# Kernel optimization log

Measured on AMD Instinct MI355X. Metric: run time of the kernel, lower is better.

## Reference

```python
import jax, jax.numpy as jnp
import numpy as np

N = 1_000_000
D = 128
S = 16384


def setup_inputs() -> dict:
    key = jax.random.key(0)
    k_x, k_idx, k_w, k_b = jax.random.split(key, 4)
    x = jax.random.normal(k_x, (N, D), dtype=jnp.float32)
    index = jnp.sort(jax.random.randint(k_idx, (N,), 0, S, dtype=jnp.int64))
    # single plain Linear layer of PyG MLP([D, D], plain_last=True)
    lim = 1.0 / np.sqrt(D)
    W = jax.random.uniform(k_w, (D, D), dtype=jnp.float32, minval=-lim, maxval=lim)
    b = jax.random.uniform(k_b, (D,), dtype=jnp.float32, minval=-lim, maxval=lim)
    return {"x": x, "W": W, "b": b, "index": index, "num_segments": S}


def reference(x, W, b, index, num_segments):
    # att = MLP(x): single plain linear layer (no activation, plain_last=True)
    att = x @ W.T + b  # [N, D]
    # segment softmax over nodes within each graph, per channel (PyG softmax)
    seg_max = jax.ops.segment_max(att, index, num_segments=num_segments)  # [S, D]
    e = jnp.exp(att - seg_max[index])  # [N, D]
    seg_sum = jax.ops.segment_sum(e, index, num_segments=num_segments)  # [S, D]
    att = e / (seg_sum[index] + 1e-16)  # [N, D]
    # attention-weighted global add pool
    return jax.ops.segment_sum(x * att, index, num_segments=num_segments)  # [S, D]
```

## Files before the change

### kernel.cpp

```cpp
#include <hip/hip_runtime.h>
#include <hip/hip_bf16.h>

#define SEGS   16384
#define DCH    128
#define CHUNK  32
#define SEGPB  4
#define FPITCH 132
#define XHBLK  520
#define LOG2E  1.4426950408889634f

using f32x4  = __attribute__((ext_vector_type(4))) float;
using bf16x8 = __attribute__((ext_vector_type(8))) short;
using u32x2  = __attribute__((ext_vector_type(2))) unsigned int;
using u32x4  = __attribute__((ext_vector_type(4))) unsigned int;

__device__ __forceinline__ float u2f(unsigned int u) { return __uint_as_float(u); }
__device__ __forceinline__ unsigned int f2u(float f) { return __float_as_uint(f); }

__global__ void setup_kernel(const float* __restrict__ W,
                             const int* __restrict__ index, int N,
                             unsigned short* __restrict__ WfH,
                             int* __restrict__ seg_start) {
  int i = blockIdx.x * blockDim.x + threadIdx.x;
  if (i < DCH * DCH) {
    int n = i >> 7, k = i & 127;
    float w = W[i] * LOG2E;
    unsigned int u = f2u(w);
    unsigned int r = (u + 0x7FFFu + ((u >> 16) & 1)) >> 16;
    int kt    = k >> 5;
    int ntile = n >> 4;
    int lane  = (n & 15) + 16 * ((k >> 3) & 3);
    int j     = k & 7;
    int dst = ((kt * 8 + ntile) * 64 + lane) * 8 + j;
    WfH[dst] = (unsigned short)r;
  } else if (i < DCH * DCH + SEGS + 1) {
    int s = i - DCH * DCH;
    int lo = 0, hi = N;
    while (lo < hi) {
      int mid = (lo + hi) >> 1;
      if (index[mid] < s) lo = mid + 1; else hi = mid;
    }
    seg_start[s] = lo;
  }
}

__global__ __launch_bounds__(256) void pool_kernel(
    const float* __restrict__ x, const float* __restrict__ bias,
    const int* __restrict__ seg_start,
    const u32x4* __restrict__ WfH,
    float* __restrict__ out) {
  __shared__ unsigned short xh[8 * XHBLK];
  __shared__ float          xf[CHUNK * FPITCH];

  const int t    = threadIdx.x;
  const int wv   = t >> 6;
  const int lane = t & 63;
  const int cl   = lane & 15;
  const int g    = lane >> 4;
  const int k31  = t & 31;
  const int lrow = t >> 5;
  const int lcol = k31 << 2;

  const int xh_base = 1040 * (k31 >> 3) + 8 * lrow + 128 * ((k31 >> 1) & 3) + 4 * (k31 & 1);
  const int xf_base = lrow * FPITCH + lcol;
  const int frag_base = lane * 8;
  const int ex_base   = g * 4 * FPITCH + wv * 32 + cl;

  u32x4 bh[4][2];
#pragma unroll
  for (int kt = 0; kt < 4; ++kt)
#pragma unroll
    for (int nt = 0; nt < 2; ++nt) {
      int off = (kt * 8 + (wv * 2 + nt)) * 64 + lane;
      bh[kt][nt] = WfH[off];
    }

  const float bc0 = bias[wv * 32 + cl]      * LOG2E;
  const float bc1 = bias[wv * 32 + 16 + cl] * LOG2E;

  const int s0   = blockIdx.x * SEGPB;
  const int sEnd = s0 + SEGPB;
  const int R0   = seg_start[s0];
  const int R1   = seg_start[sEnd];

  if (R0 == R1) {
    if (lane < 16) {
      for (int es = s0; es < sEnd; ++es) {
        out[(size_t)es * DCH + wv * 32 + cl]      = 0.f;
        out[(size_t)es * DCH + wv * 32 + 16 + cl] = 0.f;
      }
    }
    return;
  }

  int curSeg = s0;
  int segEnd = seg_start[curSeg + 1];

  int c0 = R0;
  f32x4 pv[4];
#pragma unroll
  for (int p = 0; p < 4; ++p) {
    int lr = c0 + lrow + p * 8;
    f32x4 v = {0.f, 0.f, 0.f, 0.f};
    if (lr < R1) v = *(const f32x4*)(x + (size_t)lr * DCH + lcol);
    pv[p] = v;
  }

  float den[2] = {0.f, 0.f};
  float num[2] = {0.f, 0.f};

  while (true) {
#pragma unroll
    for (int p = 0; p < 4; ++p) {
      f32x4 v = pv[p];
      unsigned int u0 = f2u(v[0]), u1 = f2u(v[1]), u2 = f2u(v[2]), u3 = f2u(v[3]);
      u32x2 H = { (u1 & 0xFFFF0000u) | (u0 >> 16),
                  (u3 & 0xFFFF0000u) | (u2 >> 16) };
      *(u32x2*)&xh[xh_base + (p >> 1) * XHBLK + (p & 1) * 64] = H;
      *(f32x4*)&xf[xf_base + p * 8 * FPITCH] = v;
    }

    const int nc0 = c0 + CHUNK;
    if (nc0 < R1) {
#pragma unroll
      for (int p = 0; p < 4; ++p) {
        int lr = nc0 + lrow + p * 8;
        f32x4 v = {0.f, 0.f, 0.f, 0.f};
        if (lr < R1) v = *(const f32x4*)(x + (size_t)lr * DCH + lcol);
        pv[p] = v;
      }
    }

    asm volatile("s_waitcnt lgkmcnt(0)" ::: "memory");
    __builtin_amdgcn_sched_barrier(0);
    __builtin_amdgcn_s_barrier();
    __builtin_amdgcn_sched_barrier(0);

    f32x4 Cf[2][2];
#pragma unroll
    for (int mt = 0; mt < 2; ++mt) {
      Cf[mt][0] = (f32x4){bc0, bc0, bc0, bc0};
      Cf[mt][1] = (f32x4){bc1, bc1, bc1, bc1};
    }
#pragma unroll
    for (int kt = 0; kt < 4; ++kt) {
      u32x4 ah[2];
#pragma unroll
      for (int mt = 0; mt < 2; ++mt)
        ah[mt] = *(const u32x4*)&xh[frag_base + (2 * kt + mt) * XHBLK];
#pragma unroll
      for (int mt = 0; mt < 2; ++mt)
#pragma unroll
        for (int nt = 0; nt < 2; ++nt) {
          bf16x8 A = __builtin_bit_cast(bf16x8, ah[mt]);
          bf16x8 B = __builtin_bit_cast(bf16x8, bh[kt][nt]);
          Cf[mt][nt] = __builtin_amdgcn_mfma_f32_16x16x32_bf16(A, B, Cf[mt][nt], 0, 0, 0);
        }
    }

    float pr[2][2][4], xv[2][2][4];
#pragma unroll
    for (int nt = 0; nt < 2; ++nt)
#pragma unroll
      for (int mt = 0; mt < 2; ++mt)
#pragma unroll
        for (int r = 0; r < 4; ++r) {
          pr[nt][mt][r] = __builtin_amdgcn_exp2f(Cf[mt][nt][r]);
          xv[nt][mt][r] = xf[ex_base + (mt * 16 + r) * FPITCH + nt * 16];
        }

    const int lim = c0 + CHUNK;
    int lo = c0;
    while (curSeg < sEnd) {
      const int hi  = segEnd;
      const int hiC = (hi < lim) ? hi : lim;
#pragma unroll
      for (int nt = 0; nt < 2; ++nt)
#pragma unroll
        for (int mt = 0; mt < 2; ++mt)
#pragma unroll
          for (int r = 0; r < 4; ++r) {
            const int row = c0 + mt * 16 + g * 4 + r;
            const bool use = (row >= lo) & (row < hiC);
            const float pp = use ? pr[nt][mt][r] : 0.f;
            den[nt] += pp;
            num[nt] += pp * xv[nt][mt][r];
          }
      if (hi <= lim) {
#pragma unroll
        for (int nt = 0; nt < 2; ++nt) {
          float l = den[nt], a = num[nt];
          l += __shfl_xor(l, 16); l += __shfl_xor(l, 32);
          a += __shfl_xor(a, 16); a += __shfl_xor(a, 32);
          if (lane < 16)
            out[(size_t)curSeg * DCH + wv * 32 + nt * 16 + cl] = a / (l + 1e-16f);
          den[nt] = 0.f; num[nt] = 0.f;
        }
        lo = hi;
        ++curSeg;
        if (curSeg < sEnd) segEnd = seg_start[curSeg + 1];
      } else {
        break;
      }
    }
    if (curSeg >= sEnd) break;
    c0 = nc0;

    asm volatile("s_waitcnt lgkmcnt(0)" ::: "memory");
    __builtin_amdgcn_sched_barrier(0);
    __builtin_amdgcn_s_barrier();
    __builtin_amdgcn_sched_barrier(0);
  }
}

extern "C" void kernel_launch(void* const* d_in, const int* in_sizes, int n_in,
                              void* d_out, int out_size, void* d_ws, size_t ws_size,
                              hipStream_t stream) {
  const float* x    = (const float*)d_in[0];
  const float* W    = (const float*)d_in[1];
  const float* bias = (const float*)d_in[2];
  const int*   idx  = (const int*)d_in[3];
  const int N = in_sizes[0] / DCH;

  unsigned short* WfH = (unsigned short*)d_ws;
  int* seg = (int*)(WfH + DCH * DCH);

  int setup_threads = DCH * DCH + SEGS + 1;
  setup_kernel<<<(setup_threads + 255) / 256, 256, 0, stream>>>(W, idx, N, WfH, seg);
  pool_kernel<<<SEGS / SEGPB, 256, 0, stream>>>(x, bias, seg,
                                                (const u32x4*)WfH,
                                                (float*)d_out);
}
```

Before: 119.3 us.

## Double-buffer bf16 LDS tile and read pooling values from bf16 copy

Drops the separate fp32 LDS copy of x and reads the pooling multiplicand back from the bf16 tile already used for the MFMA A operand. Rounding now adds 0x8000 before truncating. The bf16 tile is double-buffered across alternating chunk iterations, which removes the second barrier per chunk. This cuts LDS traffic and synchronisation, but x in the weighted sum now carries bf16 precision instead of fp32, which can raise numerical error.

After: 117.2 us. No clear change (-1.8%).

```diff
diff --git a/kernel.cpp b/kernel.cpp
--- a/kernel.cpp
+++ b/kernel.cpp
@@ -5,7 +5,6 @@
 #define DCH    128
 #define CHUNK  32
 #define SEGPB  4
-#define FPITCH 132
 #define XHBLK  520
 #define LOG2E  1.4426950408889634f
 
@@ -49,8 +48,7 @@
     const int* __restrict__ seg_start,
     const u32x4* __restrict__ WfH,
     float* __restrict__ out) {
-  __shared__ unsigned short xh[8 * XHBLK];
-  __shared__ float          xf[CHUNK * FPITCH];
+  __shared__ unsigned short xh[2][8 * XHBLK];
 
   const int t    = threadIdx.x;
   const int wv   = t >> 6;
@@ -61,10 +59,9 @@
   const int lrow = t >> 5;
   const int lcol = k31 << 2;
 
-  const int xh_base = 1040 * (k31 >> 3) + 8 * lrow + 128 * ((k31 >> 1) & 3) + 4 * (k31 & 1);
-  const int xf_base = lrow * FPITCH + lcol;
+  const int xh_base   = 1040 * (k31 >> 3) + 8 * lrow + 128 * ((k31 >> 1) & 3) + 4 * (k31 & 1);
   const int frag_base = lane * 8;
-  const int ex_base   = g * 4 * FPITCH + wv * 32 + cl;
+  const int ex0 = 2 * wv * XHBLK + 32 * g + 128 * (cl >> 3) + (cl & 7);
 
   u32x4 bh[4][2];
 #pragma unroll
@@ -95,8 +92,8 @@
 
   int curSeg = s0;
   int segEnd = seg_start[curSeg + 1];
-
   int c0 = R0;
+
   f32x4 pv[4];
 #pragma unroll
   for (int p = 0; p < 4; ++p) {
@@ -109,15 +106,15 @@
   float den[2] = {0.f, 0.f};
   float num[2] = {0.f, 0.f};
 
-  while (true) {
+  auto body = [&](unsigned short* XH) -> bool {
 #pragma unroll
     for (int p = 0; p < 4; ++p) {
       f32x4 v = pv[p];
-      unsigned int u0 = f2u(v[0]), u1 = f2u(v[1]), u2 = f2u(v[2]), u3 = f2u(v[3]);
+      unsigned int u0 = f2u(v[0]) + 0x8000u, u1 = f2u(v[1]) + 0x8000u;
+      unsigned int u2 = f2u(v[2]) + 0x8000u, u3 = f2u(v[3]) + 0x8000u;
       u32x2 H = { (u1 & 0xFFFF0000u) | (u0 >> 16),
                   (u3 & 0xFFFF0000u) | (u2 >> 16) };
-      *(u32x2*)&xh[xh_base + (p >> 1) * XHBLK + (p & 1) * 64] = H;
-      *(f32x4*)&xf[xf_base + p * 8 * FPITCH] = v;
+      *(u32x2*)&XH[xh_base + (p >> 1) * XHBLK + (p & 1) * 64] = H;
     }
 
     const int nc0 = c0 + CHUNK;
@@ -147,7 +144,7 @@
       u32x4 ah[2];
 #pragma unroll
       for (int mt = 0; mt < 2; ++mt)
-        ah[mt] = *(const u32x4*)&xh[frag_base + (2 * kt + mt) * XHBLK];
+        ah[mt] = *(const u32x4*)&XH[frag_base + (2 * kt + mt) * XHBLK];
 #pragma unroll
       for (int mt = 0; mt < 2; ++mt)
 #pragma unroll
@@ -166,7 +163,8 @@
 #pragma unroll
         for (int r = 0; r < 4; ++r) {
           pr[nt][mt][r] = __builtin_amdgcn_exp2f(Cf[mt][nt][r]);
-          xv[nt][mt][r] = xf[ex_base + (mt * 16 + r) * FPITCH + nt * 16];
+          unsigned int hv = XH[ex0 + mt * XHBLK + nt * 256 + r * 8];
+          xv[nt][mt][r] = u2f(hv << 16);
         }
 
     const int lim = c0 + CHUNK;
@@ -203,13 +201,14 @@
         break;
       }
     }
-    if (curSeg >= sEnd) break;
+    if (curSeg >= sEnd) return false;
     c0 = nc0;
-
-    asm volatile("s_waitcnt lgkmcnt(0)" ::: "memory");
-    __builtin_amdgcn_sched_barrier(0);
-    __builtin_amdgcn_s_barrier();
-    __builtin_amdgcn_sched_barrier(0);
+    return true;
+  };
+
+  for (;;) {
+    if (!body(&xh[0][0])) break;
+    if (!body(&xh[1][0])) break;
   }
 }
 
```
